# Optimization experiments

Measured on AMD Instinct MI355X. Metric: run time of the kernel, lower is better.

Reference implementation:

```python
import jax, jax.numpy as jnp
import numpy as np

DIM = 128
EDGE_FEAT_DIM = 2
N_NODES = 50000
N_EDGES = 600000
EPS = 1e-5


def setup_inputs() -> dict:
    key = jax.random.key(0)
    ks = jax.random.split(key, 16)
    d = DIM
    inp = {}
    inp["x"] = jax.random.normal(ks[0], (N_NODES, d), dtype=jnp.float32)
    inp["edge_index"] = jax.random.randint(ks[1], (2, N_EDGES), 0, N_NODES, dtype=jnp.int32)
    inp["edge_weight_norm"] = jax.random.uniform(ks[2], (N_EDGES,), dtype=jnp.float32)
    inp["edge_feat"] = jax.random.normal(ks[3], (N_EDGES, EDGE_FEAT_DIM), dtype=jnp.float32)
    inp["batch"] = jnp.zeros((N_NODES,), dtype=jnp.int32)
    # phi: Linear(dim, dim)
    inp["W_phi"] = jax.random.normal(ks[4], (d, d), dtype=jnp.float32) * (1.0 / np.sqrt(d))
    inp["b_phi"] = jnp.zeros((d,), dtype=jnp.float32)
    # edge_gate: Linear(2d+2, d) -> BN(d) -> GELU -> Linear(d, 1)
    din = 2 * d + EDGE_FEAT_DIM
    inp["W_g1"] = jax.random.normal(ks[5], (din, d), dtype=jnp.float32) * (1.0 / np.sqrt(din))
    inp["b_g1"] = jnp.zeros((d,), dtype=jnp.float32)
    inp["bn_gamma"] = jnp.ones((d,), dtype=jnp.float32)
    inp["bn_beta"] = jnp.zeros((d,), dtype=jnp.float32)
    inp["bn_mean"] = jnp.zeros((d,), dtype=jnp.float32)
    inp["bn_var"] = jnp.ones((d,), dtype=jnp.float32)
    inp["W_g2"] = jax.random.normal(ks[6], (d, 1), dtype=jnp.float32) * (1.0 / np.sqrt(d))
    inp["b_g2"] = jnp.zeros((1,), dtype=jnp.float32)
    # upd: Linear(2d, d)
    inp["W_u"] = jax.random.normal(ks[7], (2 * d, d), dtype=jnp.float32) * (1.0 / np.sqrt(2 * d))
    inp["b_u"] = jnp.zeros((d,), dtype=jnp.float32)
    # LayerNorm(dim)
    inp["ln_gamma"] = jnp.ones((d,), dtype=jnp.float32)
    inp["ln_beta"] = jnp.zeros((d,), dtype=jnp.float32)
    return inp


def reference(x, edge_index, edge_weight_norm, edge_feat, batch,
              W_phi, b_phi, W_g1, b_g1, bn_gamma, bn_beta, bn_mean, bn_var,
              W_g2, b_g2, W_u, b_u, ln_gamma, ln_beta):
    src, dst = edge_index[0], edge_index[1]
    # phi(x): [N, d]
    xj = x @ W_phi + b_phi
    # edge gate MLP on [x_dst, x_src, e]: [E, 2d+2]
    g_in = jnp.concatenate([x[dst], x[src], edge_feat], axis=-1)
    h1 = g_in @ W_g1 + b_g1
    h1 = (h1 - bn_mean) * jax.lax.rsqrt(bn_var + EPS) * bn_gamma + bn_beta  # BN eval mode
    h1 = jax.nn.gelu(h1, approximate=False)
    gate = jax.nn.sigmoid(h1 @ W_g2 + b_g2)[:, 0]  # [E]
    # messages and scatter-add aggregation
    msg = xj[src] * (edge_weight_norm * gate)[:, None]  # [E, d]
    agg = jax.ops.segment_sum(msg, dst, num_segments=x.shape[0])  # [N, d]
    # update MLP + GELU + residual + LayerNorm
    h = jnp.concatenate([x, agg], axis=-1) @ W_u + b_u
    h = jax.nn.gelu(h, approximate=False)
    y = x + h
    mu = jnp.mean(y, axis=-1, keepdims=True)
    var = jnp.var(y, axis=-1, keepdims=True)
    return (y - mu) * jax.lax.rsqrt(var + EPS) * ln_gamma + ln_beta
```

## Files before the change

### kernel.cpp

```cpp
#include <hip/hip_runtime.h>
#include <hip/hip_fp16.h>
#include <math.h>

#define DIM 128
#define NN 50000
#define NE 600000
#define EPS 1e-5f
#define CAP 64

struct H8 { __half2 h[4]; };
struct F8 { float4 a, b; };

typedef _Float16 f16x8 __attribute__((ext_vector_type(8)));
typedef float    f32x4 __attribute__((ext_vector_type(4)));

__device__ __forceinline__ float gelu_fast(float x) {
    const float c1 = 2.3022085f;
    const float c2 = 0.1029437f;
    const float x2 = x * x;
    const float z  = x * __builtin_fmaf(c2, x2, c1);
    const float u  = __builtin_amdgcn_exp2f(z);
    const float r  = __builtin_amdgcn_rcpf(1.f + u);
    return __builtin_fmaf(-x, r, x);
}

__device__ __forceinline__ float sigmoid_fast(float y) {
    const float u = __builtin_amdgcn_exp2f(-1.4426950409f * y);
    return __builtin_amdgcn_rcpf(1.f + u);
}

__global__ __launch_bounds__(256) void k_prep_scale(
    const float* __restrict__ Wg1, const float* __restrict__ bg1,
    const float* __restrict__ bng, const float* __restrict__ bnb,
    const float* __restrict__ bnm, const float* __restrict__ bnv,
    __half* __restrict__ WABth, float* __restrict__ bA,
    float* __restrict__ w0p, float* __restrict__ w1p)
{
    const int k = blockIdx.x;
    const int t = threadIdx.x;
    const int c = t & 127;
    const float s = bng[c] * rsqrtf(bnv[c] + EPS);
    const float w = (t < 128) ? Wg1[k * DIM + c] : Wg1[(DIM + k) * DIM + c];
    WABth[t * DIM + k] = __float2half(w * s);
    if (k == 0 && t < 128) {
        const float tt = bnb[c] - bnm[c] * s;
        bA[c]  = bg1[c] * s + tt;
        w0p[c] = Wg1[256 * DIM + c] * s;
        w1p[c] = Wg1[257 * DIM + c] * s;
    }
}

__global__ __launch_bounds__(128) void k_prep_wpu(
    const float* __restrict__ Wphi, const float* __restrict__ bphi,
    const float* __restrict__ Wu,
    __half* __restrict__ Wct, float* __restrict__ bpu)
{
    const int a = blockIdx.x;
    const int j = threadIdx.x;
    float acc = 0.f;
    #pragma unroll 8
    for (int k = 0; k < DIM; ++k)
        acc += Wphi[a * DIM + k] * Wu[(DIM + k) * DIM + j];
    Wct[j * 256 + a]       = __float2half(Wu[a * DIM + j]);
    Wct[j * 256 + 128 + a] = __float2half(acc);
    if (a == 0) {
        float b = 0.f;
        #pragma unroll 8
        for (int k = 0; k < DIM; ++k)
            b += bphi[k] * Wu[(DIM + k) * DIM + j];
        bpu[j] = b;
    }
}

__global__ __launch_bounds__(256) void k_node_mfma(
    const float* __restrict__ x, const __half* __restrict__ WABth,
    const float* __restrict__ bA,
    __half* __restrict__ A, __half* __restrict__ Bv, __half* __restrict__ xh)
{
    __shared__ __half tile[64][264];
    const int t    = threadIdx.x;
    const int wv   = t >> 6;
    const int lane = t & 63;
    const int n16  = lane & 15;
    const int quad = lane >> 4;
    const int m0   = blockIdx.x * 64;

    f32x4 acc[4][4];
    #pragma unroll
    for (int mt = 0; mt < 4; ++mt)
        #pragma unroll
        for (int nt = 0; nt < 4; ++nt)
            acc[mt][nt] = (f32x4){0.f, 0.f, 0.f, 0.f};

    int rowm[4];
    #pragma unroll
    for (int mt = 0; mt < 4; ++mt)
        rowm[mt] = min(m0 + mt * 16 + n16, NN - 1);

    #pragma unroll
    for (int ks = 0; ks < 4; ++ks) {
        const int ko = ks * 32 + quad * 8;
        f16x8 bf[4];
        #pragma unroll
        for (int nt = 0; nt < 4; ++nt) {
            const int c = wv * 64 + nt * 16 + n16;
            bf[nt] = *(const f16x8*)(WABth + c * DIM + ko);
        }
        #pragma unroll
        for (int mt = 0; mt < 4; ++mt) {
            const float4 xa = *(const float4*)(x + (size_t)rowm[mt] * DIM + ko);
            const float4 xb = *(const float4*)(x + (size_t)rowm[mt] * DIM + ko + 4);
            f16x8 af;
            af[0] = (_Float16)xa.x; af[1] = (_Float16)xa.y;
            af[2] = (_Float16)xa.z; af[3] = (_Float16)xa.w;
            af[4] = (_Float16)xb.x; af[5] = (_Float16)xb.y;
            af[6] = (_Float16)xb.z; af[7] = (_Float16)xb.w;
            if (wv == 0)
                *(f16x8*)(xh + (size_t)rowm[mt] * DIM + ko) = af;
            #pragma unroll
            for (int nt = 0; nt < 4; ++nt)
                acc[mt][nt] = __builtin_amdgcn_mfma_f32_16x16x32_f16(
                    af, bf[nt], acc[mt][nt], 0, 0, 0);
        }
    }

    #pragma unroll
    for (int nt = 0; nt < 4; ++nt) {
        const int c = wv * 64 + nt * 16 + n16;
        const float bias = (c < 128) ? bA[c] : 0.f;
        #pragma unroll
        for (int mt = 0; mt < 4; ++mt)
            #pragma unroll
            for (int reg = 0; reg < 4; ++reg)
                tile[mt * 16 + quad * 4 + reg][c] =
                    __float2half(acc[mt][nt][reg] + bias);
    }
    __syncthreads();

    #pragma unroll
    for (int i = 0; i < 8; ++i) {
        const int chunk = t + i * 256;
        const int row = chunk >> 5;
        const int o   = (chunk & 31) * 8;
        if (m0 + row < NN) {
            const uint4 v = *(const uint4*)&tile[row][o];
            if (o < 128) *(uint4*)(A  + (size_t)(m0 + row) * DIM + o)       = v;
            else         *(uint4*)(Bv + (size_t)(m0 + row) * DIM + o - 128) = v;
        }
    }
}

__global__ __launch_bounds__(256) void k_gate(
    const int*   __restrict__ ei,  const float* __restrict__ ew,
    const float* __restrict__ ef,
    const __half* __restrict__ A,  const __half* __restrict__ Bv,
    const float* __restrict__ w0p, const float* __restrict__ w1p,
    const float* __restrict__ Wg2, const float* __restrict__ bg2,
    int* __restrict__ deg, int2* __restrict__ pairs)
{
    const int t    = threadIdx.x;
    const int lane = t & 63;
    const int sub  = lane >> 4;
    const int sl   = lane & 15;
    const int c8   = sl * 8;
    const int e0   = (blockIdx.x * 4 + (t >> 6)) * 8 + sub * 2;

    const F8 WG = *(const F8*)(Wg2 + c8);
    const F8 W0 = *(const F8*)(w0p + c8);
    const F8 W1 = *(const F8*)(w1p + c8);
    const float bg2v = bg2[0];
    const float* w0 = (const float*)&W0;
    const float* w1 = (const float*)&W1;
    const float* wg = (const float*)&WG;

    const int2   srcs = *(const int2*)(ei + e0);
    const int2   dsts = *(const int2*)(ei + NE + e0);
    const float4 efv  = *(const float4*)(ef + 2 * e0);
    const float2 ewv  = *(const float2*)(ew + e0);

    const H8 a0 = *(const H8*)(A  + (size_t)dsts.x * DIM + c8);
    const H8 b0 = *(const H8*)(Bv + (size_t)srcs.x * DIM + c8);
    const H8 a1 = *(const H8*)(A  + (size_t)dsts.y * DIM + c8);
    const H8 b1 = *(const H8*)(Bv + (size_t)srcs.y * DIM + c8);

    float p0 = 0.f, p1 = 0.f;
    #pragma unroll
    for (int i = 0; i < 4; ++i) {
        const float2 s0 = __half22float2(__hadd2(a0.h[i], b0.h[i]));
        const float2 s1 = __half22float2(__hadd2(a1.h[i], b1.h[i]));
        const int c0 = 2 * i, c1 = 2 * i + 1;
        float h;
        h = s0.x + efv.x * w0[c0] + efv.y * w1[c0];
        p0 = __builtin_fmaf(gelu_fast(h), wg[c0], p0);
        h = s0.y + efv.x * w0[c1] + efv.y * w1[c1];
        p0 = __builtin_fmaf(gelu_fast(h), wg[c1], p0);
        h = s1.x + efv.z * w0[c0] + efv.w * w1[c0];
        p1 = __builtin_fmaf(gelu_fast(h), wg[c0], p1);
        h = s1.y + efv.z * w0[c1] + efv.w * w1[c1];
        p1 = __builtin_fmaf(gelu_fast(h), wg[c1], p1);
    }
    #pragma unroll
    for (int off = 1; off < 16; off <<= 1) {
        p0 += __shfl_xor(p0, off, 64);
        p1 += __shfl_xor(p1, off, 64);
    }

    if (sl == 0) {
        const float coef0 = ewv.x * sigmoid_fast(p0 + bg2v);
        const float coef1 = ewv.y * sigmoid_fast(p1 + bg2v);
        const int pos0 = atomicAdd(&deg[dsts.x], 1);
        if (pos0 < CAP)
            pairs[(size_t)dsts.x * CAP + pos0] = make_int2(srcs.x, __float_as_int(coef0));
        const int pos1 = atomicAdd(&deg[dsts.y], 1);
        if (pos1 < CAP)
            pairs[(size_t)dsts.y * CAP + pos1] = make_int2(srcs.y, __float_as_int(coef1));
    }
}

__global__ __launch_bounds__(64, 3) void k_agg_update(
    const int* __restrict__ deg, const int2* __restrict__ pairs,
    const __half* __restrict__ xh, const __half* __restrict__ Wct,
    const float* __restrict__ bu, const float* __restrict__ bpu,
    const float* __restrict__ lng, const float* __restrict__ lnb,
    float* __restrict__ out)
{
    __shared__ __half xt[16][136];
    __shared__ __half at[16][136];
    __shared__ float sct[16];

    const int t    = threadIdx.x;
    const int n16  = t & 15;
    const int quad = t >> 4;
    const int m0   = blockIdx.x * 16;

    const int slot = t >> 4;
    const int sl   = t & 15;
    const int c8   = sl * 8;

    int    dd[4];
    size_t bb[4];
    #pragma unroll
    for (int r = 0; r < 4; ++r) {
        const int lr = r * 4 + slot;
        const int nc = min(m0 + lr, NN - 1);
        dd[r] = min(deg[nc], CAP);
        bb[r] = (size_t)nc * CAP;
    }

    #pragma unroll
    for (int i = 0; i < 4; ++i) {
        const int idx = i * 64 + t;
        const int row = idx >> 4;
        const int col = (idx & 15) * 8;
        const int grow = min(m0 + row, NN - 1);
        *(f16x8*)&xt[row][col] = *(const f16x8*)(xh + (size_t)grow * DIM + col);
    }

    float acc[4][8];
    float scn[4] = {0.f, 0.f, 0.f, 0.f};
    #pragma unroll
    for (int r = 0; r < 4; ++r)
        #pragma unroll
        for (int i = 0; i < 8; ++i) acc[r][i] = 0.f;

    const int dmax = max(max(dd[0], dd[1]), max(dd[2], dd[3]));

    for (int j = 0; j < dmax; j += 4) {
        int4 pq0[4], pq1[4];
        #pragma unroll
        for (int r = 0; r < 4; ++r) {
            pq0[r] = *(const int4*)(&pairs[bb[r] + j]);
            pq1[r] = *(const int4*)(&pairs[bb[r] + j + 2]);
        }

        int   ix[16];
        float cf[16];
        #pragma unroll
        for (int r = 0; r < 4; ++r) {
            const int q = 4 * r;
            const bool v0 = (j     < dd[r]);
            const bool v1 = (j + 1 < dd[r]);
            const bool v2 = (j + 2 < dd[r]);
            const bool v3 = (j + 3 < dd[r]);
            ix[q]     = v0 ? pq0[r].x : 0;
            cf[q]     = v0 ? __int_as_float(pq0[r].y) : 0.f;
            ix[q + 1] = v1 ? pq0[r].z : 0;
            cf[q + 1] = v1 ? __int_as_float(pq0[r].w) : 0.f;
            ix[q + 2] = v2 ? pq1[r].x : 0;
            cf[q + 2] = v2 ? __int_as_float(pq1[r].y) : 0.f;
            ix[q + 3] = v3 ? pq1[r].z : 0;
            cf[q + 3] = v3 ? __int_as_float(pq1[r].w) : 0.f;
        }

        H8 xv[16];
        #pragma unroll
        for (int q = 0; q < 16; ++q)
            xv[q] = *(const H8*)(xh + (size_t)ix[q] * DIM + c8);

        #pragma unroll
        for (int r = 0; r < 4; ++r) {
            #pragma unroll
            for (int k = 0; k < 4; ++k) {
                const int   q = 4 * r + k;
                const float c = cf[q];
                #pragma unroll
                for (int i = 0; i < 4; ++i) {
                    const float2 f = __half22float2(xv[q].h[i]);
                    acc[r][2 * i]     = __builtin_fmaf(c, f.x, acc[r][2 * i]);
                    acc[r][2 * i + 1] = __builtin_fmaf(c, f.y, acc[r][2 * i + 1]);
                }
                scn[r] += c;
            }
        }
    }

    #pragma unroll
    for (int r = 0; r < 4; ++r) {
        const int lr = r * 4 + slot;
        f16x8 hv;
        #pragma unroll
        for (int i = 0; i < 8; ++i) hv[i] = (_Float16)acc[r][i];
        *(f16x8*)&at[lr][c8] = hv;
        if (sl == 0) sct[lr] = scn[r];
    }
    __syncthreads();

    f32x4 acc2[8];
    #pragma unroll
    for (int nt = 0; nt < 8; ++nt) acc2[nt] = (f32x4){0.f, 0.f, 0.f, 0.f};

    const int rloc = n16;
    #pragma unroll
    for (int ks = 0; ks < 4; ++ks) {
        const int ko = ks * 32 + quad * 8;
        const f16x8 af = *(const f16x8*)&xt[rloc][ko];
        #pragma unroll
        for (int nt = 0; nt < 8; ++nt) {
            const f16x8 bf = *(const f16x8*)(Wct + (nt * 16 + n16) * 256 + ko);
            acc2[nt] = __builtin_amdgcn_mfma_f32_16x16x32_f16(af, bf, acc2[nt], 0, 0, 0);
        }
    }
    #pragma unroll
    for (int ks = 0; ks < 4; ++ks) {
        const int ko = ks * 32 + quad * 8;
        const f16x8 af = *(const f16x8*)&at[rloc][ko];
        #pragma unroll
        for (int nt = 0; nt < 8; ++nt) {
            const f16x8 bf = *(const f16x8*)(Wct + (nt * 16 + n16) * 256 + 128 + ko);
            acc2[nt] = __builtin_amdgcn_mfma_f32_16x16x32_f16(af, bf, acc2[nt], 0, 0, 0);
        }
    }

    int   rl[4];
    float scv[4];
    #pragma unroll
    for (int reg = 0; reg < 4; ++reg) {
        rl[reg]  = quad * 4 + reg;
        scv[reg] = sct[rl[reg]];
    }

    float yv[8][4];
    float s[4]  = {0.f, 0.f, 0.f, 0.f};
    float ss[4] = {0.f, 0.f, 0.f, 0.f};

    #pragma unroll
    for (int nt = 0; nt < 8; ++nt) {
        const int c = nt * 16 + n16;
        const float buv = bu[c], bpv = bpu[c];
        #pragma unroll
        for (int reg = 0; reg < 4; ++reg) {
            float h = acc2[nt][reg] + buv + scv[reg] * bpv;
            h = gelu_fast(h);
            const float xv = __half2float(xt[rl[reg]][c]);
            const float y = xv + h;
            yv[nt][reg] = y;
            s[reg]  += y;
            ss[reg] += y * y;
        }
    }

    #pragma unroll
    for (int reg = 0; reg < 4; ++reg) {
        #pragma unroll
        for (int off = 1; off < 16; off <<= 1) {
            s[reg]  += __shfl_xor(s[reg],  off, 64);
            ss[reg] += __shfl_xor(ss[reg], off, 64);
        }
    }

    float mu[4], rs[4];
    #pragma unroll
    for (int reg = 0; reg < 4; ++reg) {
        mu[reg] = s[reg] * (1.f / DIM);
        const float var = ss[reg] * (1.f / DIM) - mu[reg] * mu[reg];
        rs[reg] = rsqrtf(var + EPS);
    }

    #pragma unroll
    for (int nt = 0; nt < 8; ++nt) {
        const int c = nt * 16 + n16;
        const float gg = lng[c], bb2 = lnb[c];
        #pragma unroll
        for (int reg = 0; reg < 4; ++reg) {
            const int grow = m0 + rl[reg];
            if (grow < NN)
                __builtin_nontemporal_store(
                    (yv[nt][reg] - mu[reg]) * rs[reg] * gg + bb2,
                    &out[(size_t)grow * DIM + c]);
        }
    }
}

extern "C" void kernel_launch(void* const* d_in, const int* in_sizes, int n_in,
                              void* d_out, int out_size, void* d_ws, size_t ws_size,
                              hipStream_t stream)
{
    const float* x    = (const float*)d_in[0];
    const int*   ei   = (const int*)  d_in[1];
    const float* ew   = (const float*)d_in[2];
    const float* ef   = (const float*)d_in[3];
    const float* Wphi = (const float*)d_in[5];
    const float* bphi = (const float*)d_in[6];
    const float* Wg1  = (const float*)d_in[7];
    const float* bg1  = (const float*)d_in[8];
    const float* bng  = (const float*)d_in[9];
    const float* bnb  = (const float*)d_in[10];
    const float* bnm  = (const float*)d_in[11];
    const float* bnv  = (const float*)d_in[12];
    const float* Wg2  = (const float*)d_in[13];
    const float* bg2  = (const float*)d_in[14];
    const float* Wu   = (const float*)d_in[15];
    const float* bu   = (const float*)d_in[16];
    const float* lng  = (const float*)d_in[17];
    const float* lnb  = (const float*)d_in[18];

    float* out = (float*)d_out;

    char* wsb = (char*)d_ws;
    size_t off = 0;
    auto carve = [&](size_t bytes) -> void* {
        void* p = wsb + off;
        off += (bytes + 255) & ~(size_t)255;
        return p;
    };
    __half* xh    = (__half*)carve((size_t)NN * DIM * 2);
    __half* A     = (__half*)carve((size_t)NN * DIM * 2);
    __half* Bv    = (__half*)carve((size_t)NN * DIM * 2);
    __half* WABth = (__half*)carve(256 * DIM * 2);
    __half* Wct   = (__half*)carve(DIM * 256 * 2);
    float*  bA    = (float*) carve(DIM * 4);
    float*  w0p   = (float*) carve(DIM * 4);
    float*  w1p   = (float*) carve(DIM * 4);
    float*  bpu   = (float*) carve(DIM * 4);
    int*    deg   = (int*)   carve((size_t)NN * 4);
    int2*   pairs = (int2*)  carve((size_t)NN * CAP * 8 + 256);

    hipMemsetAsync(deg, 0, (size_t)NN * 4, stream);

    k_prep_scale<<<128, 256, 0, stream>>>(Wg1, bg1, bng, bnb, bnm, bnv,
                                          WABth, bA, w0p, w1p);
    k_prep_wpu<<<128, 128, 0, stream>>>(Wphi, bphi, Wu, Wct, bpu);
    k_node_mfma<<<(NN + 63) / 64, 256, 0, stream>>>(x, WABth, bA, A, Bv, xh);
    k_gate<<<NE / 32, 256, 0, stream>>>(ei, ew, ef, A, Bv, w0p, w1p, Wg2, bg2,
                                        deg, pairs);
    k_agg_update<<<(NN + 15) / 16, 64, 0, stream>>>(deg, pairs, xh, Wct,
                                                    bu, bpu, lng, lnb, out);
}
```

Before: 263.6 us.

## Fuse edge gate into aggregation, bucket edges alongside node GEMM, interleave Bv/xh

Removes the separate edge-gate kernel. The node GEMM kernel gets extra blocks that bucket edges by destination, storing (src, edge id) pairs. The aggregation kernel now computes the gate per edge in place, using the destination's A row and the source's interleaved Bv/xh row, so one 512-byte row fetch serves both the gate and the message. This saves a kernel launch and one scatter of pairs. In exchange, edge weights and features are fetched indirectly, each iteration handles fewer edges (2 instead of 4), and register pressure rises in a kernel limited to 64 threads.

```diff
diff --git a/kernel.cpp b/kernel.cpp
--- a/kernel.cpp
+++ b/kernel.cpp
@@ -7,6 +7,8 @@
 #define NE 600000
 #define EPS 1e-5f
 #define CAP 64
+#define NB_NODE 782
+#define NB_EDGE 586
 
 struct H8 { __half2 h[4]; };
 struct F8 { float4 a, b; };
@@ -72,12 +74,31 @@
     }
 }
 
-__global__ __launch_bounds__(256) void k_node_mfma(
+__global__ __launch_bounds__(256) void k_node_bucket(
     const float* __restrict__ x, const __half* __restrict__ WABth,
     const float* __restrict__ bA,
-    __half* __restrict__ A, __half* __restrict__ Bv, __half* __restrict__ xh)
+    const int* __restrict__ ei,
+    __half* __restrict__ A, __half* __restrict__ BX,
+    int* __restrict__ deg, int2* __restrict__ pairs)
 {
     __shared__ __half tile[64][264];
+
+    if (blockIdx.x >= NB_NODE) {
+        const int tid = (blockIdx.x - NB_NODE) * 256 + threadIdx.x;
+        #pragma unroll
+        for (int k = 0; k < 4; ++k) {
+            const int e = tid + k * (NB_EDGE * 256);
+            if (e < NE) {
+                const int s = ei[e];
+                const int d = ei[NE + e];
+                const int pos = atomicAdd(&deg[d], 1);
+                if (pos < CAP)
+                    pairs[(size_t)d * CAP + pos] = make_int2(s, e);
+            }
+        }
+        return;
+    }
+
     const int t    = threadIdx.x;
     const int wv   = t >> 6;
     const int lane = t & 63;
@@ -116,7 +137,7 @@
             af[4] = (_Float16)xb.x; af[5] = (_Float16)xb.y;
             af[6] = (_Float16)xb.z; af[7] = (_Float16)xb.w;
             if (wv == 0)
-                *(f16x8*)(xh + (size_t)rowm[mt] * DIM + ko) = af;
+                *(f16x8*)(BX + (size_t)rowm[mt] * 256 + 2 * ko + 8) = af;
             #pragma unroll
             for (int nt = 0; nt < 4; ++nt)
                 acc[mt][nt] = __builtin_amdgcn_mfma_f32_16x16x32_f16(
@@ -144,82 +165,21 @@
         const int o   = (chunk & 31) * 8;
         if (m0 + row < NN) {
             const uint4 v = *(const uint4*)&tile[row][o];
-            if (o < 128) *(uint4*)(A  + (size_t)(m0 + row) * DIM + o)       = v;
-            else         *(uint4*)(Bv + (size_t)(m0 + row) * DIM + o - 128) = v;
-        }
-    }
-}
-
-__global__ __launch_bounds__(256) void k_gate(
-    const int*   __restrict__ ei,  const float* __restrict__ ew,
-    const float* __restrict__ ef,
-    const __half* __restrict__ A,  const __half* __restrict__ Bv,
+            if (o < 128)
+                *(uint4*)(A + (size_t)(m0 + row) * DIM + o) = v;
+            else
+                *(uint4*)(BX + (size_t)(m0 + row) * 256 + 2 * (o - 128)) = v;
+        }
+    }
+}
+
+__global__ __launch_bounds__(64, 3) void k_agg_update(
+    const int* __restrict__ deg, const int2* __restrict__ pairs,
+    const __half* __restrict__ A, const __half* __restrict__ BX,
+    const float* __restrict__ ew, const float* __restrict__ ef,
+    const __half* __restrict__ Wct,
     const float* __restrict__ w0p, const float* __restrict__ w1p,
     const float* __restrict__ Wg2, const float* __restrict__ bg2,
-    int* __restrict__ deg, int2* __restrict__ pairs)
-{
-    const int t    = threadIdx.x;
-    const int lane = t & 63;
-    const int sub  = lane >> 4;
-    const int sl   = lane & 15;
-    const int c8   = sl * 8;
-    const int e0   = (blockIdx.x * 4 + (t >> 6)) * 8 + sub * 2;
-
-    const F8 WG = *(const F8*)(Wg2 + c8);
-    const F8 W0 = *(const F8*)(w0p + c8);
-    const F8 W1 = *(const F8*)(w1p + c8);
-    const float bg2v = bg2[0];
-    const float* w0 = (const float*)&W0;
-    const float* w1 = (const float*)&W1;
-    const float* wg = (const float*)&WG;
-
-    const int2   srcs = *(const int2*)(ei + e0);
-    const int2   dsts = *(const int2*)(ei + NE + e0);
-    const float4 efv  = *(const float4*)(ef + 2 * e0);
-    const float2 ewv  = *(const float2*)(ew + e0);
-
-    const H8 a0 = *(const H8*)(A  + (size_t)dsts.x * DIM + c8);
-    const H8 b0 = *(const H8*)(Bv + (size_t)srcs.x * DIM + c8);
-    const H8 a1 = *(const H8*)(A  + (size_t)dsts.y * DIM + c8);
-    const H8 b1 = *(const H8*)(Bv + (size_t)srcs.y * DIM + c8);
-
-    float p0 = 0.f, p1 = 0.f;
-    #pragma unroll
-    for (int i = 0; i < 4; ++i) {
-        const float2 s0 = __half22float2(__hadd2(a0.h[i], b0.h[i]));
-        const float2 s1 = __half22float2(__hadd2(a1.h[i], b1.h[i]));
-        const int c0 = 2 * i, c1 = 2 * i + 1;
-        float h;
-        h = s0.x + efv.x * w0[c0] + efv.y * w1[c0];
-        p0 = __builtin_fmaf(gelu_fast(h), wg[c0], p0);
-        h = s0.y + efv.x * w0[c1] + efv.y * w1[c1];
-        p0 = __builtin_fmaf(gelu_fast(h), wg[c1], p0);
-        h = s1.x + efv.z * w0[c0] + efv.w * w1[c0];
-        p1 = __builtin_fmaf(gelu_fast(h), wg[c0], p1);
-        h = s1.y + efv.z * w0[c1] + efv.w * w1[c1];
-        p1 = __builtin_fmaf(gelu_fast(h), wg[c1], p1);
-    }
-    #pragma unroll
-    for (int off = 1; off < 16; off <<= 1) {
-        p0 += __shfl_xor(p0, off, 64);
-        p1 += __shfl_xor(p1, off, 64);
-    }
-
-    if (sl == 0) {
-        const float coef0 = ewv.x * sigmoid_fast(p0 + bg2v);
-        const float coef1 = ewv.y * sigmoid_fast(p1 + bg2v);
-        const int pos0 = atomicAdd(&deg[dsts.x], 1);
-        if (pos0 < CAP)
-            pairs[(size_t)dsts.x * CAP + pos0] = make_int2(srcs.x, __float_as_int(coef0));
-        const int pos1 = atomicAdd(&deg[dsts.y], 1);
-        if (pos1 < CAP)
-            pairs[(size_t)dsts.y * CAP + pos1] = make_int2(srcs.y, __float_as_int(coef1));
-    }
-}
-
-__global__ __launch_bounds__(64, 3) void k_agg_update(
-    const int* __restrict__ deg, const int2* __restrict__ pairs,
-    const __half* __restrict__ xh, const __half* __restrict__ Wct,
     const float* __restrict__ bu, const float* __restrict__ bpu,
     const float* __restrict__ lng, const float* __restrict__ lnb,
     float* __restrict__ out)
@@ -233,27 +193,38 @@
     const int quad = t >> 4;
     const int m0   = blockIdx.x * 16;
 
-    const int slot = t >> 4;
-    const int sl   = t & 15;
+    const int slot = quad;
+    const int sl   = n16;
     const int c8   = sl * 8;
 
     int    dd[4];
     size_t bb[4];
+    H8     arow[4];
     #pragma unroll
     for (int r = 0; r < 4; ++r) {
         const int lr = r * 4 + slot;
         const int nc = min(m0 + lr, NN - 1);
         dd[r] = min(deg[nc], CAP);
         bb[r] = (size_t)nc * CAP;
-    }
+        arow[r] = *(const H8*)(A + (size_t)nc * DIM + c8);
+    }
+
+    const F8 W0 = *(const F8*)(w0p + c8);
+    const F8 W1 = *(const F8*)(w1p + c8);
+    const F8 WG = *(const F8*)(Wg2 + c8);
+    const float bg2v = bg2[0];
+    const float* w0 = (const float*)&W0;
+    const float* w1 = (const float*)&W1;
+    const float* wg = (const float*)&WG;
 
     #pragma unroll
     for (int i = 0; i < 4; ++i) {
         const int idx = i * 64 + t;
         const int row = idx >> 4;
-        const int col = (idx & 15) * 8;
+        const int cb  = idx & 15;
         const int grow = min(m0 + row, NN - 1);
-        *(f16x8*)&xt[row][col] = *(const f16x8*)(xh + (size_t)grow * DIM + col);
+        *(f16x8*)&xt[row][cb * 8] =
+            *(const f16x8*)(BX + (size_t)grow * 256 + cb * 16 + 8);
     }
 
     float acc[4][8];
@@ -265,52 +236,71 @@
 
     const int dmax = max(max(dd[0], dd[1]), max(dd[2], dd[3]));
 
-    for (int j = 0; j < dmax; j += 4) {
-        int4 pq0[4], pq1[4];
+    for (int j = 0; j < dmax; j += 2) {
+        int   ixs[8], eid[8];
+        float vld[8];
         #pragma unroll
         for (int r = 0; r < 4; ++r) {
-            pq0[r] = *(const int4*)(&pairs[bb[r] + j]);
-            pq1[r] = *(const int4*)(&pairs[bb[r] + j + 2]);
-        }
-
-        int   ix[16];
-        float cf[16];
-        #pragma unroll
-        for (int r = 0; r < 4; ++r) {
-            const int q = 4 * r;
+            const int4 pq = *(const int4*)(&pairs[bb[r] + j]);
             const bool v0 = (j     < dd[r]);
             const bool v1 = (j + 1 < dd[r]);
-            const bool v2 = (j + 2 < dd[r]);
-            const bool v3 = (j + 3 < dd[r]);
-            ix[q]     = v0 ? pq0[r].x : 0;
-            cf[q]     = v0 ? __int_as_float(pq0[r].y) : 0.f;
-            ix[q + 1] = v1 ? pq0[r].z : 0;
-            cf[q + 1] = v1 ? __int_as_float(pq0[r].w) : 0.f;
-            ix[q + 2] = v2 ? pq1[r].x : 0;
-            cf[q + 2] = v2 ? __int_as_float(pq1[r].y) : 0.f;
-            ix[q + 3] = v3 ? pq1[r].z : 0;
-            cf[q + 3] = v3 ? __int_as_float(pq1[r].w) : 0.f;
-        }
-
-        H8 xv[16];
-        #pragma unroll
-        for (int q = 0; q < 16; ++q)
-            xv[q] = *(const H8*)(xh + (size_t)ix[q] * DIM + c8);
-
-        #pragma unroll
-        for (int r = 0; r < 4; ++r) {
+            ixs[2 * r]     = v0 ? pq.x : 0;
+            eid[2 * r]     = v0 ? pq.y : 0;
+            vld[2 * r]     = v0 ? 1.f : 0.f;
+            ixs[2 * r + 1] = v1 ? pq.z : 0;
+            eid[2 * r + 1] = v1 ? pq.w : 0;
+            vld[2 * r + 1] = v1 ? 1.f : 0.f;
+        }
+
+        f16x8  bv[8];
+        float2 efv[8];
+        float  eww[8];
+        #pragma unroll
+        for (int q = 0; q < 8; ++q) {
+            bv[q]  = *(const f16x8*)(BX + (size_t)ixs[q] * 256 + sl * 16);
+            efv[q] = *(const float2*)(ef + 2 * eid[q]);
+            eww[q] = ew[eid[q]] * vld[q];
+        }
+
+        float coef[8];
+        #pragma unroll
+        for (int q = 0; q < 8; ++q) {
+            const int r = q >> 1;
+            const H8& bh = (const H8&)bv[q];
+            float p = 0.f;
             #pragma unroll
-            for (int k = 0; k < 4; ++k) {
-                const int   q = 4 * r + k;
-                const float c = cf[q];
-                #pragma unroll
-                for (int i = 0; i < 4; ++i) {
-                    const float2 f = __half22float2(xv[q].h[i]);
-                    acc[r][2 * i]     = __builtin_fmaf(c, f.x, acc[r][2 * i]);
-                    acc[r][2 * i + 1] = __builtin_fmaf(c, f.y, acc[r][2 * i + 1]);
-                }
-                scn[r] += c;
+            for (int i = 0; i < 4; ++i) {
+                const float2 sum = __half22float2(__hadd2(arow[r].h[i], bh.h[i]));
+                const int c0 = 2 * i, c1 = 2 * i + 1;
+                float h;
+                h = sum.x + efv[q].x * w0[c0] + efv[q].y * w1[c0];
+                p = __builtin_fmaf(gelu_fast(h), wg[c0], p);
+                h = sum.y + efv[q].x * w0[c1] + efv[q].y * w1[c1];
+                p = __builtin_fmaf(gelu_fast(h), wg[c1], p);
             }
+            #pragma unroll
+            for (int off = 1; off < 16; off <<= 1)
+                p += __shfl_xor(p, off, 64);
+            coef[q] = eww[q] * sigmoid_fast(p + bg2v);
+        }
+
+        f16x8 xv[8];
+        #pragma unroll
+        for (int q = 0; q < 8; ++q)
+            xv[q] = *(const f16x8*)(BX + (size_t)ixs[q] * 256 + sl * 16 + 8);
+
+        #pragma unroll
+        for (int q = 0; q < 8; ++q) {
+            const int r = q >> 1;
+            const float c = coef[q];
+            const H8& xx = (const H8&)xv[q];
+            #pragma unroll
+            for (int i = 0; i < 4; ++i) {
+                const float2 f = __half22float2(xx.h[i]);
+                acc[r][2 * i]     = __builtin_fmaf(c, f.x, acc[r][2 * i]);
+                acc[r][2 * i + 1] = __builtin_fmaf(c, f.y, acc[r][2 * i + 1]);
+            }
+            scn[r] += c;
         }
     }
 
@@ -443,9 +433,8 @@
         off += (bytes + 255) & ~(size_t)255;
         return p;
     };
-    __half* xh    = (__half*)carve((size_t)NN * DIM * 2);
     __half* A     = (__half*)carve((size_t)NN * DIM * 2);
-    __half* Bv    = (__half*)carve((size_t)NN * DIM * 2);
+    __half* BX    = (__half*)carve((size_t)NN * 256 * 2);
     __half* WABth = (__half*)carve(256 * DIM * 2);
     __half* Wct   = (__half*)carve(DIM * 256 * 2);
     float*  bA    = (float*) carve(DIM * 4);
@@ -460,9 +449,9 @@
     k_prep_scale<<<128, 256, 0, stream>>>(Wg1, bg1, bng, bnb, bnm, bnv,
                                           WABth, bA, w0p, w1p);
     k_prep_wpu<<<128, 128, 0, stream>>>(Wphi, bphi, Wu, Wct, bpu);
-    k_node_mfma<<<(NN + 63) / 64, 256, 0, stream>>>(x, WABth, bA, A, Bv, xh);
-    k_gate<<<NE / 32, 256, 0, stream>>>(ei, ew, ef, A, Bv, w0p, w1p, Wg2, bg2,
-                                        deg, pairs);
-    k_agg_update<<<(NN + 15) / 16, 64, 0, stream>>>(deg, pairs, xh, Wct,
-                                                    bu, bpu, lng, lnb, out);
-}
+    k_node_bucket<<<NB_NODE + NB_EDGE, 256, 0, stream>>>(
+        x, WABth, bA, ei, A, BX, deg, pairs);
+    k_agg_update<<<(NN + 15) / 16, 64, 0, stream>>>(
+        deg, pairs, A, BX, ew, ef, Wct, w0p, w1p, Wg2, bg2,
+        bu, bpu, lng, lnb, out);
+}
```

Result: slower. 371.2 us (+40.8%).

## Split per-node aggregation and update GEMM across two wavefronts per block

Applied to the files above, without the earlier changes.

The aggregation/update kernel now runs two wavefronts per 16-node block. Each wave gathers half of each node's edge list into its own shared partial buffer. The update GEMM sums both partials through the K dimension, with each wave computing 64 of the 128 output columns. LayerNorm statistics are combined across the waves via shared memory plus an extra barrier. The aim is more memory-level parallelism and shorter per-wave gather chains, at the cost of doubling the A-side MFMA work and adding shared-memory traffic and synchronization.

```diff
diff --git a/kernel.cpp b/kernel.cpp
--- a/kernel.cpp
+++ b/kernel.cpp
@@ -217,7 +217,7 @@
     }
 }
 
-__global__ __launch_bounds__(64, 3) void k_agg_update(
+__global__ __launch_bounds__(128, 3) void k_agg_update(
     const int* __restrict__ deg, const int2* __restrict__ pairs,
     const __half* __restrict__ xh, const __half* __restrict__ Wct,
     const float* __restrict__ bu, const float* __restrict__ bpu,
@@ -225,31 +225,39 @@
     float* __restrict__ out)
 {
     __shared__ __half xt[16][136];
-    __shared__ __half at[16][136];
-    __shared__ float sct[16];
+    __shared__ __half at[2][16][136];
+    __shared__ float  sct[2][16];
+    __shared__ float  sred_s[2][16];
+    __shared__ float  sred_ss[2][16];
 
     const int t    = threadIdx.x;
-    const int n16  = t & 15;
-    const int quad = t >> 4;
+    const int w    = t >> 6;
+    const int lane = t & 63;
+    const int n16  = lane & 15;
+    const int quad = lane >> 4;
     const int m0   = blockIdx.x * 16;
 
-    const int slot = t >> 4;
-    const int sl   = t & 15;
+    const int slot = quad;
+    const int sl   = n16;
     const int c8   = sl * 8;
 
-    int    dd[4];
-    size_t bb[4];
+    int    cnt[4];
+    size_t pb[4];
     #pragma unroll
     for (int r = 0; r < 4; ++r) {
         const int lr = r * 4 + slot;
         const int nc = min(m0 + lr, NN - 1);
-        dd[r] = min(deg[nc], CAP);
-        bb[r] = (size_t)nc * CAP;
-    }
-
-    #pragma unroll
-    for (int i = 0; i < 4; ++i) {
-        const int idx = i * 64 + t;
+        const int d  = min(deg[nc], CAP);
+        const int h  = ((d + 2) >> 2) << 1;
+        const int lo = w ? h : 0;
+        const int hi = w ? d : h;
+        cnt[r] = hi - lo;
+        pb[r]  = (size_t)nc * CAP + lo;
+    }
+
+    #pragma unroll
+    for (int i = 0; i < 2; ++i) {
+        const int idx = i * 128 + t;
         const int row = idx >> 4;
         const int col = (idx & 15) * 8;
         const int grow = min(m0 + row, NN - 1);
@@ -263,14 +271,14 @@
         #pragma unroll
         for (int i = 0; i < 8; ++i) acc[r][i] = 0.f;
 
-    const int dmax = max(max(dd[0], dd[1]), max(dd[2], dd[3]));
-
-    for (int j = 0; j < dmax; j += 4) {
+    const int cmax = max(max(cnt[0], cnt[1]), max(cnt[2], cnt[3]));
+
+    for (int jj = 0; jj < cmax; jj += 4) {
         int4 pq0[4], pq1[4];
         #pragma unroll
         for (int r = 0; r < 4; ++r) {
-            pq0[r] = *(const int4*)(&pairs[bb[r] + j]);
-            pq1[r] = *(const int4*)(&pairs[bb[r] + j + 2]);
+            pq0[r] = *(const int4*)(&pairs[pb[r] + jj]);
+            pq1[r] = *(const int4*)(&pairs[pb[r] + jj + 2]);
         }
 
         int   ix[16];
@@ -278,10 +286,10 @@
         #pragma unroll
         for (int r = 0; r < 4; ++r) {
             const int q = 4 * r;
-            const bool v0 = (j     < dd[r]);
-            const bool v1 = (j + 1 < dd[r]);
-            const bool v2 = (j + 2 < dd[r]);
-            const bool v3 = (j + 3 < dd[r]);
+            const bool v0 = (jj     < cnt[r]);
+            const bool v1 = (jj + 1 < cnt[r]);
+            const bool v2 = (jj + 2 < cnt[r]);
+            const bool v3 = (jj + 3 < cnt[r]);
             ix[q]     = v0 ? pq0[r].x : 0;
             cf[q]     = v0 ? __int_as_float(pq0[r].y) : 0.f;
             ix[q + 1] = v1 ? pq0[r].z : 0;
@@ -320,14 +328,14 @@
         f16x8 hv;
         #pragma unroll
         for (int i = 0; i < 8; ++i) hv[i] = (_Float16)acc[r][i];
-        *(f16x8*)&at[lr][c8] = hv;
-        if (sl == 0) sct[lr] = scn[r];
+        *(f16x8*)&at[w][lr][c8] = hv;
+        if (sl == 0) sct[w][lr] = scn[r];
     }
     __syncthreads();
 
-    f32x4 acc2[8];
-    #pragma unroll
-    for (int nt = 0; nt < 8; ++nt) acc2[nt] = (f32x4){0.f, 0.f, 0.f, 0.f};
+    f32x4 acc2[4];
+    #pragma unroll
+    for (int nt = 0; nt < 4; ++nt) acc2[nt] = (f32x4){0.f, 0.f, 0.f, 0.f};
 
     const int rloc = n16;
     #pragma unroll
@@ -335,19 +343,24 @@
         const int ko = ks * 32 + quad * 8;
         const f16x8 af = *(const f16x8*)&xt[rloc][ko];
         #pragma unroll
-        for (int nt = 0; nt < 8; ++nt) {
-            const f16x8 bf = *(const f16x8*)(Wct + (nt * 16 + n16) * 256 + ko);
+        for (int nt = 0; nt < 4; ++nt) {
+            const int c = w * 64 + nt * 16 + n16;
+            const f16x8 bf = *(const f16x8*)(Wct + c * 256 + ko);
             acc2[nt] = __builtin_amdgcn_mfma_f32_16x16x32_f16(af, bf, acc2[nt], 0, 0, 0);
         }
     }
     #pragma unroll
-    for (int ks = 0; ks < 4; ++ks) {
-        const int ko = ks * 32 + quad * 8;
-        const f16x8 af = *(const f16x8*)&at[rloc][ko];
-        #pragma unroll
-        for (int nt = 0; nt < 8; ++nt) {
-            const f16x8 bf = *(const f16x8*)(Wct + (nt * 16 + n16) * 256 + 128 + ko);
-            acc2[nt] = __builtin_amdgcn_mfma_f32_16x16x32_f16(af, bf, acc2[nt], 0, 0, 0);
+    for (int half = 0; half < 2; ++half) {
+        #pragma unroll
+        for (int ks = 0; ks < 4; ++ks) {
+            const int ko = ks * 32 + quad * 8;
+            const f16x8 af = *(const f16x8*)&at[half][rloc][ko];
+            #pragma unroll
+            for (int nt = 0; nt < 4; ++nt) {
+                const int c = w * 64 + nt * 16 + n16;
+                const f16x8 bf = *(const f16x8*)(Wct + c * 256 + 128 + ko);
+                acc2[nt] = __builtin_amdgcn_mfma_f32_16x16x32_f16(af, bf, acc2[nt], 0, 0, 0);
+            }
         }
     }
 
@@ -356,16 +369,16 @@
     #pragma unroll
     for (int reg = 0; reg < 4; ++reg) {
         rl[reg]  = quad * 4 + reg;
-        scv[reg] = sct[rl[reg]];
-    }
-
-    float yv[8][4];
+        scv[reg] = sct[0][rl[reg]] + sct[1][rl[reg]];
+    }
+
+    float yv[4][4];
     float s[4]  = {0.f, 0.f, 0.f, 0.f};
     float ss[4] = {0.f, 0.f, 0.f, 0.f};
 
     #pragma unroll
-    for (int nt = 0; nt < 8; ++nt) {
-        const int c = nt * 16 + n16;
+    for (int nt = 0; nt < 4; ++nt) {
+        const int c = w * 64 + nt * 16 + n16;
         const float buv = bu[c], bpv = bpu[c];
         #pragma unroll
         for (int reg = 0; reg < 4; ++reg) {
@@ -387,18 +400,28 @@
             ss[reg] += __shfl_xor(ss[reg], off, 64);
         }
     }
+    if (n16 == 0) {
+        #pragma unroll
+        for (int reg = 0; reg < 4; ++reg) {
+            sred_s[w][rl[reg]]  = s[reg];
+            sred_ss[w][rl[reg]] = ss[reg];
+        }
+    }
+    __syncthreads();
 
     float mu[4], rs[4];
     #pragma unroll
     for (int reg = 0; reg < 4; ++reg) {
-        mu[reg] = s[reg] * (1.f / DIM);
-        const float var = ss[reg] * (1.f / DIM) - mu[reg] * mu[reg];
+        const float stot  = sred_s[0][rl[reg]]  + sred_s[1][rl[reg]];
+        const float sstot = sred_ss[0][rl[reg]] + sred_ss[1][rl[reg]];
+        mu[reg] = stot * (1.f / DIM);
+        const float var = sstot * (1.f / DIM) - mu[reg] * mu[reg];
         rs[reg] = rsqrtf(var + EPS);
     }
 
     #pragma unroll
-    for (int nt = 0; nt < 8; ++nt) {
-        const int c = nt * 16 + n16;
+    for (int nt = 0; nt < 4; ++nt) {
+        const int c = w * 64 + nt * 16 + n16;
         const float gg = lng[c], bb2 = lnb[c];
         #pragma unroll
         for (int reg = 0; reg < 4; ++reg) {
@@ -463,6 +486,6 @@
     k_node_mfma<<<(NN + 63) / 64, 256, 0, stream>>>(x, WABth, bA, A, Bv, xh);
     k_gate<<<NE / 32, 256, 0, stream>>>(ei, ew, ef, A, Bv, w0p, w1p, Wg2, bg2,
                                         deg, pairs);
-    k_agg_update<<<(NN + 15) / 16, 64, 0, stream>>>(deg, pairs, xh, Wct,
-                                                    bu, bpu, lng, lnb, out);
-}
+    k_agg_update<<<(NN + 15) / 16, 128, 0, stream>>>(deg, pairs, xh, Wct,
+                                                     bu, bpu, lng, lnb, out);
+}
```

After: 269.3 us. 2.2% more time.
